# Kernel optimization log

Hardware: AMD Instinct MI355X
Metric: run time of the kernel (lower is better)

## Reference

```python
import jax, jax.numpy as jnp
import numpy as np

NUM_NODES = 10000
IN_DIM = 128
GAT_UNITS = 64
K = 20  # min(20, num_nodes - 1)
NEG_SLOPE = 0.2


def setup_inputs() -> dict:
    key = jax.random.key(0)
    ks = jax.random.split(key, 10)
    s = lambda k, shape, scale: jax.random.normal(k, shape, jnp.float32) * scale
    return {
        "x": s(ks[0], (NUM_NODES, IN_DIM), 1.0),
        "emb": s(ks[1], (NUM_NODES, 16), 1.0),
        "W1": s(ks[2], (IN_DIM, 4, GAT_UNITS), 0.05),
        "a1_src": s(ks[3], (4, GAT_UNITS), 0.05),
        "a1_tgt": s(ks[4], (4, GAT_UNITS), 0.05),
        "b1": jnp.zeros((4 * GAT_UNITS,), jnp.float32),
        "W2": s(ks[5], (4 * GAT_UNITS, 1, GAT_UNITS), 0.05),
        "a2_src": s(ks[6], (1, GAT_UNITS), 0.05),
        "a2_tgt": s(ks[7], (1, GAT_UNITS), 0.05),
        "b2": jnp.zeros((GAT_UNITS,), jnp.float32),
    }


def _build_edges(emb):
    # top-k adjacency from cosine similarity of node embeddings
    norm = emb / jnp.linalg.norm(emb, axis=-1, keepdims=True)
    sim = norm @ norm.T                      # [N, N]
    _, idx = jax.lax.top_k(sim, K)           # [N, K]
    n = emb.shape[0]
    src = jnp.repeat(jnp.arange(n, dtype=jnp.int32), K)
    tgt = idx.reshape(-1).astype(jnp.int32)
    # append self loops (as in the original module)
    loop = jnp.arange(n, dtype=jnp.int32)
    src = jnp.concatenate([src, loop])
    tgt = jnp.concatenate([tgt, loop])
    return src, tgt                          # each [N*(K+1)]


def _gat(x, W, a_src, a_tgt, src, tgt, n):
    # x: [N, F]; W: [F, H, C]; a_*: [H, C]
    h = jnp.einsum("nf,fhc->nhc", x, W)      # [N, H, C]
    e_src = jnp.einsum("nhc,hc->nh", h, a_src)  # [N, H]
    e_tgt = jnp.einsum("nhc,hc->nh", h, a_tgt)  # [N, H]
    logits = jax.nn.leaky_relu(e_src[src] + e_tgt[tgt], NEG_SLOPE)  # [E, H]
    # segment softmax over each source node's neighborhood
    m = jax.ops.segment_max(logits, src, num_segments=n)
    ex = jnp.exp(logits - m[src])
    z = jax.ops.segment_sum(ex, src, num_segments=n)
    alpha = ex / z[src]                      # [E, H]
    msg = alpha[:, :, None] * h[tgt]         # [E, H, C]
    return jax.ops.segment_sum(msg, src, num_segments=n)  # [N, H, C]


def reference(x, emb, W1, a1_src, a1_tgt, b1, W2, a2_src, a2_tgt, b2):
    n = x.shape[0]
    src, tgt = _build_edges(emb)
    # GAT layer 1: 4 heads, concatenated
    h1 = _gat(x, W1, a1_src, a1_tgt, src, tgt, n)        # [N, 4, C]
    h1 = h1.reshape(n, -1) + b1                           # [N, 4C]
    h1 = jax.nn.relu(h1)                                  # (dropout: inference mode)
    # GAT layer 2: 1 head, no concat
    h2 = _gat(h1, W2, a2_src, a2_tgt, src, tgt, n)        # [N, 1, C]
    return h2[:, 0, :] + b2                               # [N, C]
```

## Files before the change

kernel.cpp:

```cpp
#include <hip/hip_runtime.h>
#include <math.h>


#define N_NODES 10000
#define EMB_D   16
#define IN_DIM  128
#define H1      4
#define CDIM    64
#define D1      256
#define K_TOP   20
#define NEIGH   21
#define SROWS   32
#define NTILES  313
#define JSPLIT  2
#define HALFT   160
#define CAPM    96
#define GUARD   0.016f

typedef __attribute__((ext_vector_type(8)))  short short8;
typedef __attribute__((ext_vector_type(16))) float f32x16;

__device__ __forceinline__ unsigned monokey(float v) {
  unsigned u = __float_as_uint(v);
  return (u & 0x80000000u) ? ~u : (u | 0x80000000u);
}
__device__ __forceinline__ float invmono(unsigned m) {
  unsigned u = (m & 0x80000000u) ? (m ^ 0x80000000u) : ~m;
  return __uint_as_float(u);
}
__device__ __forceinline__ unsigned short f32_to_bf16(float f) {
  unsigned u = __float_as_uint(f);
  unsigned r = 0x7FFFu + ((u >> 16) & 1u);
  return (unsigned short)((u + r) >> 16);
}

__device__ __forceinline__ float dot16q(float4 qa, float4 qb, float4 qc, float4 qd,
                                        float4 v0, float4 v1, float4 v2, float4 v3) {
  float a = 0.f;
  a = fmaf(qa.x, v0.x, a); a = fmaf(qa.y, v0.y, a);
  a = fmaf(qa.z, v0.z, a); a = fmaf(qa.w, v0.w, a);
  a = fmaf(qb.x, v1.x, a); a = fmaf(qb.y, v1.y, a);
  a = fmaf(qb.z, v1.z, a); a = fmaf(qb.w, v1.w, a);
  a = fmaf(qc.x, v2.x, a); a = fmaf(qc.y, v2.y, a);
  a = fmaf(qc.z, v2.z, a); a = fmaf(qc.w, v2.w, a);
  a = fmaf(qd.x, v3.x, a); a = fmaf(qd.y, v3.y, a);
  a = fmaf(qd.z, v3.z, a); a = fmaf(qd.w, v3.w, a);
  return a;
}

__global__ __launch_bounds__(256) void normalize_kernel(
    const float* __restrict__ emb, float* __restrict__ nrm,
    unsigned short* __restrict__ nrmh) {
  int i = blockIdx.x * 256 + threadIdx.x;
  if (i >= N_NODES) return;
  const float4* p = (const float4*)(emb + (size_t)i * EMB_D);
  float4 v[4];
  float ss = 0.f;
#pragma unroll
  for (int k = 0; k < 4; k++) {
    v[k] = p[k];
    ss = fmaf(v[k].x, v[k].x, ss);
    ss = fmaf(v[k].y, v[k].y, ss);
    ss = fmaf(v[k].z, v[k].z, ss);
    ss = fmaf(v[k].w, v[k].w, ss);
  }
  float nv = sqrtf(ss);
  float4* o = (float4*)(nrm + (size_t)i * EMB_D);
  ushort4* oh = (ushort4*)(nrmh + (size_t)i * EMB_D);
#pragma unroll
  for (int k = 0; k < 4; k++) {
    float4 t;
    t.x = v[k].x / nv; t.y = v[k].y / nv; t.z = v[k].z / nv; t.w = v[k].w / nv;
    o[k] = t;
    ushort4 h;
    h.x = f32_to_bf16(t.x); h.y = f32_to_bf16(t.y);
    h.z = f32_to_bf16(t.z); h.w = f32_to_bf16(t.w);
    oh[k] = h;
  }
}

__global__ __launch_bounds__(512) void sim_topk_part(
    const float* __restrict__ nrm, const unsigned short* __restrict__ nrmh,
    unsigned long long* __restrict__ pkeys) {
  __shared__ unsigned short s_qbf[SROWS * EMB_D];
  __shared__ float s_qf[SROWS * EMB_D];
  __shared__ __align__(16) char s_ovl[32768];
  float (*s_smax)[256] = (float(*)[256])s_ovl;
  unsigned long long (*s_ckey)[CAPM] = (unsigned long long(*)[CAPM])s_ovl;
  unsigned short (*s_cid)[CAPM] =
      (unsigned short(*)[CAPM])(s_ovl + 24576);
  __shared__ float s_thr[SROWS];
  __shared__ int s_cnt[SROWS];

  int tid = threadIdx.x;
  int w = tid >> 6, lane = tid & 63;
  int lo5 = lane & 31, hi = lane >> 5;
  int row0 = blockIdx.x * SROWS;
  int bh = blockIdx.y;
  int tbase = bh * HALFT;

  if (tid < SROWS * EMB_D) {
    int gi = row0 * EMB_D + tid;
    float v = (gi < N_NODES * EMB_D) ? nrm[gi] : 0.f;
    s_qf[tid] = v;
    s_qbf[tid] = f32_to_bf16(v);
  }
  if (tid < SROWS) s_cnt[tid] = 0;
  __syncthreads();

  short8 afrag = *(const short8*)&s_qbf[lo5 * EMB_D + hi * 8];
  const f32x16 zacc = (f32x16)0.0f;

  float rm[16];
#pragma unroll
  for (int r = 0; r < 16; r++) rm[r] = -INFINITY;

#pragma unroll
  for (int g = 0; g < 5; ++g) {
    int tb = tbase + g * 32 + w * 4;
    int nd[4];
    short8 bf[4];
#pragma unroll
    for (int u = 0; u < 4; u++) {
      nd[u] = (tb + u) * 32 + lo5;
      bf[u] = (short8)(short)0;
      if (nd[u] < N_NODES)
        bf[u] = *(const short8*)&nrmh[(size_t)nd[u] * EMB_D + hi * 8];
    }
#pragma unroll
    for (int u = 0; u < 4; u++) {
      f32x16 acc = __builtin_amdgcn_mfma_f32_32x32x16_bf16(afrag, bf[u], zacc, 0, 0, 0);
      if (nd[u] < N_NODES) {
#pragma unroll
        for (int r = 0; r < 16; r++) rm[r] = fmaxf(rm[r], acc[r]);
      }
    }
  }
#pragma unroll
  for (int r = 0; r < 16; r++) {
    int rl = (r & 3) + 8 * (r >> 2) + 4 * hi;
    s_smax[rl][w * 32 + lo5] = rm[r];
  }
  __syncthreads();

  for (int q = 0; q < 4; q++) {
    int row = w * 4 + q;
    float m01 = fmaxf(s_smax[row][lane], s_smax[row][64 + lane]);
    float m23 = fmaxf(s_smax[row][128 + lane], s_smax[row][192 + lane]);
    unsigned v = monokey(fmaxf(m01, m23));
#pragma unroll
    for (int k = 2; k <= 64; k <<= 1) {
#pragma unroll
      for (int j = k >> 1; j > 0; j >>= 1) {
        unsigned o = __shfl_xor(v, j);
        bool upper = (lane & j) != 0;
        bool ascend = (lane & k) == 0;
        unsigned mx = v > o ? v : o;
        unsigned mn = v > o ? o : v;
        v = (upper == ascend) ? mx : mn;
      }
    }
    unsigned t20 = __shfl(v, 44);
    if (lane == 0)
      s_thr[row] = (row0 + row < N_NODES) ? invmono(t20) - GUARD : INFINITY;
  }
  __syncthreads();

  float thr_r[16];
#pragma unroll
  for (int r = 0; r < 16; r++)
    thr_r[r] = s_thr[(r & 3) + 8 * (r >> 2) + 4 * hi];

#pragma unroll
  for (int g = 0; g < 5; ++g) {
    int tb = tbase + g * 32 + w * 4;
    int nd[4];
    short8 bf[4];
#pragma unroll
    for (int u = 0; u < 4; u++) {
      nd[u] = (tb + u) * 32 + lo5;
      bf[u] = (short8)(short)0;
      if (nd[u] < N_NODES)
        bf[u] = *(const short8*)&nrmh[(size_t)nd[u] * EMB_D + hi * 8];
    }
#pragma unroll
    for (int u = 0; u < 4; u++) {
      f32x16 acc = __builtin_amdgcn_mfma_f32_32x32x16_bf16(afrag, bf[u], zacc, 0, 0, 0);
      if (nd[u] < N_NODES) {
#pragma unroll
        for (int r = 0; r < 16; r++) {
          if (acc[r] >= thr_r[r]) {
            int rl = (r & 3) + 8 * (r >> 2) + 4 * hi;
            int slot = atomicAdd(&s_cnt[rl], 1);
            if (slot < CAPM) s_cid[rl][slot] = (unsigned short)nd[u];
          }
        }
      }
    }
  }
  __syncthreads();

  for (int q = 0; q < 4; q++) {
    int row = w * 4 + q;
    if (row0 + row >= N_NODES) continue;
    int M = s_cnt[row];
    if (M > CAPM) continue;
    const float4* qp = (const float4*)&s_qf[row * EMB_D];
    float4 qa = qp[0], qb = qp[1], qc = qp[2], qd = qp[3];
    for (int c = lane; c < M; c += 64) {
      int id = s_cid[row][c];
      const float4* pj = (const float4*)(nrm + (size_t)id * EMB_D);
      float sim = dot16q(qa, qb, qc, qd, pj[0], pj[1], pj[2], pj[3]);
      s_ckey[row][c] = ((unsigned long long)monokey(sim) << 32) |
                       (unsigned long long)(0xFFFFFFFFu - (unsigned)id);
    }
  }
  __syncthreads();

  for (int q = 0; q < 4; q++) {
    int row = w * 4 + q;
    int grow = row0 + row;
    if (grow >= N_NODES) continue;
    unsigned long long* outp = pkeys + ((size_t)grow * JSPLIT + bh) * K_TOP;
    int M = s_cnt[row];
    if (M <= CAPM) {
      for (int c = lane; c < M; c += 64) {
        unsigned long long mykey = s_ckey[row][c];
        int rank = 0;
        for (int i = 0; i < M; i++) rank += (s_ckey[row][i] > mykey) ? 1 : 0;
        if (rank < K_TOP) outp[rank] = mykey;
      }
    } else {
      const float4* qp = (const float4*)&s_qf[row * EMB_D];
      float4 qa = qp[0], qb = qp[1], qc = qp[2], qd = qp[3];
      int j0 = tbase * 32;
      int jend = j0 + HALFT * 32; if (jend > N_NODES) jend = N_NODES;
      unsigned long long prev = ~0ull;
      for (int r = 0; r < K_TOP; r++) {
        unsigned long long best = 0ull;
        for (int j = j0 + lane; j < jend; j += 64) {
          const float4* pj = (const float4*)(nrm + (size_t)j * EMB_D);
          float sim = dot16q(qa, qb, qc, qd, pj[0], pj[1], pj[2], pj[3]);
          unsigned long long key = ((unsigned long long)monokey(sim) << 32) |
                                   (unsigned long long)(0xFFFFFFFFu - (unsigned)j);
          if (key < prev && key > best) best = key;
        }
#pragma unroll
        for (int off = 32; off > 0; off >>= 1) {
          unsigned long long o = __shfl_down(best, off);
          if (o > best) best = o;
        }
        best = __shfl(best, 0);
        prev = best;
        if (lane == 0) outp[r] = best;
      }
    }
  }
}

__global__ __launch_bounds__(256) void topk_merge(
    const unsigned long long* __restrict__ pkeys, int* __restrict__ topk) {
  __shared__ unsigned long long s_k[4][JSPLIT * K_TOP];
  int w = threadIdx.x >> 6, lane = threadIdx.x & 63;
  int row = blockIdx.x * 4 + w;
  const unsigned long long* src = pkeys + (size_t)row * (JSPLIT * K_TOP);
  if (lane < JSPLIT * K_TOP) s_k[w][lane] = src[lane];
  __syncthreads();
  if (lane < JSPLIT * K_TOP) {
    unsigned long long mykey = s_k[w][lane];
    int rank = 0;
    for (int i = 0; i < JSPLIT * K_TOP; i++)
      rank += (s_k[w][i] > mykey) ? 1 : 0;
    if (rank < K_TOP)
      topk[(size_t)row * K_TOP + rank] =
          (int)(0xFFFFFFFFu - (unsigned)(mykey & 0xFFFFFFFFull));
  }
}

__global__ __launch_bounds__(256) void gemm1_kernel(
    const float* __restrict__ A, const float* __restrict__ B,
    const float* __restrict__ a_src, const float* __restrict__ a_tgt,
    float* __restrict__ Cc, float* __restrict__ es, float* __restrict__ et) {
  __shared__ float As[16][IN_DIM];
  int r0 = blockIdx.x * 16;
  int tid = threadIdx.x;
  {
    int rr = tid >> 4;
    int kk = tid & 15;
    ((float4*)&As[rr][0])[kk] = ((const float4*)(A + (size_t)(r0 + rr) * IN_DIM))[kk];
    ((float4*)&As[rr][0])[kk + 16] =
        ((const float4*)(A + (size_t)(r0 + rr) * IN_DIM))[kk + 16];
  }
  __syncthreads();
  int y = tid >> 7;
  int c0 = (tid & 127) * 2;
  float acc[8][2] = {};
  for (int k4 = 0; k4 < IN_DIM / 4; k4++) {
    float4 a[8];
#pragma unroll
    for (int r = 0; r < 8; r++) a[r] = ((const float4*)&As[y * 8 + r][0])[k4];
    float2 bv[4];
#pragma unroll
    for (int i = 0; i < 4; i++)
      bv[i] = *(const float2*)&B[(size_t)(k4 * 4 + i) * D1 + c0];
#pragma unroll
    for (int r = 0; r < 8; r++) {
      acc[r][0] = fmaf(a[r].x, bv[0].x, acc[r][0]);
      acc[r][1] = fmaf(a[r].x, bv[0].y, acc[r][1]);
      acc[r][0] = fmaf(a[r].y, bv[1].x, acc[r][0]);
      acc[r][1] = fmaf(a[r].y, bv[1].y, acc[r][1]);
      acc[r][0] = fmaf(a[r].z, bv[2].x, acc[r][0]);
      acc[r][1] = fmaf(a[r].z, bv[2].y, acc[r][1]);
      acc[r][0] = fmaf(a[r].w, bv[3].x, acc[r][0]);
      acc[r][1] = fmaf(a[r].w, bv[3].y, acc[r][1]);
    }
  }
#pragma unroll
  for (int r = 0; r < 8; r++) {
    float2 o = {acc[r][0], acc[r][1]};
    *(float2*)&Cc[(size_t)(r0 + y * 8 + r) * D1 + c0] = o;
  }
  int lane = tid & 63;
  int h = c0 >> 6;
  float as0 = a_src[c0], as1 = a_src[c0 + 1];
  float at0 = a_tgt[c0], at1 = a_tgt[c0 + 1];
#pragma unroll
  for (int r = 0; r < 8; r++) {
    float ps = fmaf(acc[r][1], as1, acc[r][0] * as0);
    float pt = fmaf(acc[r][1], at1, acc[r][0] * at0);
#pragma unroll
    for (int off = 16; off > 0; off >>= 1) {
      ps += __shfl_down(ps, off);
      pt += __shfl_down(pt, off);
    }
    if ((lane & 31) == 0) {
      es[(size_t)(r0 + y * 8 + r) * H1 + h] = ps;
      et[(size_t)(r0 + y * 8 + r) * H1 + h] = pt;
    }
  }
}

__global__ __launch_bounds__(256) void agg1_gemm2_kernel(
    const float* __restrict__ h1p, const float* __restrict__ e1s,
    const float* __restrict__ e1t, const int* __restrict__ topk,
    const float* __restrict__ b1, const float* __restrict__ B2,
    const float* __restrict__ a_src, const float* __restrict__ a_tgt,
    float* __restrict__ h2p, float* __restrict__ es, float* __restrict__ et) {
  __shared__ float As[16][D1];
  __shared__ int nb[16][NEIGH];
  __shared__ float wv[16][NEIGH][H1];
  __shared__ float zz[16][H1];
  int r0 = blockIdx.x * 16;
  int tid = threadIdx.x;

  for (int idx = tid; idx < 16 * NEIGH; idx += 256) {
    int n = idx / NEIGH, jj = idx % NEIGH;
    nb[n][jj] = (jj < K_TOP) ? topk[(size_t)(r0 + n) * K_TOP + jj] : (r0 + n);
  }
  __syncthreads();
  for (int idx = tid; idx < 16 * NEIGH * H1; idx += 256) {
    int e = idx & 3, jj = (idx >> 2) % NEIGH, n = idx / (NEIGH * H1);
    float L = e1s[(size_t)(r0 + n) * H1 + e] + e1t[(size_t)nb[n][jj] * H1 + e];
    wv[n][jj][e] = (L > 0.f) ? L : 0.2f * L;
  }
  __syncthreads();
  if (tid < 16 * H1) {
    int n = tid >> 2, h = tid & 3;
    float m = -INFINITY;
#pragma unroll
    for (int jj = 0; jj < NEIGH; jj++) m = fmaxf(m, wv[n][jj][h]);
    float z = 0.f;
#pragma unroll
    for (int jj = 0; jj < NEIGH; jj++) {
      float wt = expf(wv[n][jj][h] - m);
      z += wt;
      wv[n][jj][h] = wt;
    }
    zz[n][h] = z;
  }
  __syncthreads();
  {
    int h = tid >> 6;
    float bv = b1[tid];
    for (int n = 0; n < 16; n++) {
      float acc = 0.f;
#pragma unroll
      for (int jj = 0; jj < NEIGH; jj++)
        acc = fmaf(wv[n][jj][h], h1p[(size_t)nb[n][jj] * D1 + tid], acc);
      float o = acc / zz[n][h] + bv;
      As[n][tid] = fmaxf(o, 0.f);
    }
  }
  __syncthreads();
  int col = tid & 63, y = tid >> 6;
  float acc4[4] = {0, 0, 0, 0};
  for (int k4 = 0; k4 < D1 / 4; k4++) {
    float4 a[4];
#pragma unroll
    for (int r = 0; r < 4; r++) a[r] = ((const float4*)&As[y * 4 + r][0])[k4];
    float bv[4];
#pragma unroll
    for (int i = 0; i < 4; i++) bv[i] = B2[(size_t)(k4 * 4 + i) * CDIM + col];
#pragma unroll
    for (int r = 0; r < 4; r++) {
      acc4[r] = fmaf(a[r].x, bv[0], acc4[r]);
      acc4[r] = fmaf(a[r].y, bv[1], acc4[r]);
      acc4[r] = fmaf(a[r].z, bv[2], acc4[r]);
      acc4[r] = fmaf(a[r].w, bv[3], acc4[r]);
    }
  }
#pragma unroll
  for (int r = 0; r < 4; r++)
    h2p[(size_t)(r0 + y * 4 + r) * CDIM + col] = acc4[r];
  float as = a_src[col], at = a_tgt[col];
#pragma unroll
  for (int r = 0; r < 4; r++) {
    float ps = acc4[r] * as, pt = acc4[r] * at;
#pragma unroll
    for (int off = 32; off > 0; off >>= 1) {
      ps += __shfl_down(ps, off);
      pt += __shfl_down(pt, off);
    }
    if (col == 0) {
      es[r0 + y * 4 + r] = ps;
      et[r0 + y * 4 + r] = pt;
    }
  }
}

__global__ __launch_bounds__(256) void agg2_kernel(
    const float* __restrict__ h2p, const float* __restrict__ es,
    const float* __restrict__ et, const int* __restrict__ topk,
    const float* __restrict__ b2, float* __restrict__ out) {
  int tid = threadIdx.x;
  int li = tid >> 6;
  int c = tid & 63;
  int i = blockIdx.x * 4 + li;
  __shared__ int nb[4][NEIGH];
  __shared__ float lg[4][NEIGH];
  if (tid < 4 * NEIGH) {
    int li2 = tid / NEIGH, jj = tid % NEIGH;
    int node = blockIdx.x * 4 + li2;
    nb[li2][jj] = (jj < K_TOP) ? topk[(size_t)node * K_TOP + jj] : node;
  }
  __syncthreads();
  if (tid < 4 * NEIGH) {
    int li2 = tid / NEIGH, jj = tid % NEIGH;
    int node = blockIdx.x * 4 + li2;
    float L = es[node] + et[nb[li2][jj]];
    lg[li2][jj] = (L > 0.f) ? L : 0.2f * L;
  }
  __syncthreads();
  float m = -INFINITY;
#pragma unroll
  for (int jj = 0; jj < NEIGH; jj++) m = fmaxf(m, lg[li][jj]);
  float z = 0.f, acc = 0.f;
#pragma unroll
  for (int jj = 0; jj < NEIGH; jj++) {
    float w = expf(lg[li][jj] - m);
    z += w;
    acc = fmaf(w, h2p[(size_t)nb[li][jj] * CDIM + c], acc);
  }
  out[(size_t)i * CDIM + c] = acc / z + b2[c];
}

extern "C" void kernel_launch(void* const* d_in, const int* in_sizes, int n_in,
                              void* d_out, int out_size, void* d_ws, size_t ws_size,
                              hipStream_t stream) {
  const float* x   = (const float*)d_in[0];
  const float* emb = (const float*)d_in[1];
  const float* W1  = (const float*)d_in[2];
  const float* a1s = (const float*)d_in[3];
  const float* a1t = (const float*)d_in[4];
  const float* b1  = (const float*)d_in[5];
  const float* W2  = (const float*)d_in[6];
  const float* a2s = (const float*)d_in[7];
  const float* a2t = (const float*)d_in[8];
  const float* b2  = (const float*)d_in[9];
  float* out = (float*)d_out;

  size_t off = 0;
  auto alloc = [&](size_t bytes) {
    void* p = (char*)d_ws + off;
    off += (bytes + 255) & ~(size_t)255;
    return p;
  };
  float*          nrm  = (float*)alloc((size_t)N_NODES * EMB_D * sizeof(float));
  unsigned short* nrmh = (unsigned short*)alloc((size_t)N_NODES * EMB_D * sizeof(unsigned short));
  int*   topk = (int*)  alloc((size_t)N_NODES * K_TOP * sizeof(int));
  float* h1p  = (float*)alloc((size_t)N_NODES * D1 * sizeof(float));
  float* e1s  = (float*)alloc((size_t)N_NODES * H1 * sizeof(float));
  float* e1t  = (float*)alloc((size_t)N_NODES * H1 * sizeof(float));
  float* h2p  = (float*)alloc((size_t)N_NODES * CDIM * sizeof(float));
  float* e2s  = (float*)alloc((size_t)N_NODES * sizeof(float));
  float* e2t  = (float*)alloc((size_t)N_NODES * sizeof(float));
  unsigned long long* pkeys = (unsigned long long*)h1p;
  (void)ws_size; (void)in_sizes; (void)n_in; (void)out_size;

  normalize_kernel<<<(N_NODES + 255) / 256, 256, 0, stream>>>(emb, nrm, nrmh);
  sim_topk_part<<<dim3(NTILES, JSPLIT), 512, 0, stream>>>(nrm, nrmh, pkeys);
  topk_merge<<<N_NODES / 4, 256, 0, stream>>>(pkeys, topk);
  gemm1_kernel<<<N_NODES / 16, 256, 0, stream>>>(x, W1, a1s, a1t, h1p, e1s, e1t);
  agg1_gemm2_kernel<<<N_NODES / 16, 256, 0, stream>>>(h1p, e1s, e1t, topk, b1,
                                                      W2, a2s, a2t, h2p, e2s, e2t);
  agg2_kernel<<<N_NODES / 4, 256, 0, stream>>>(h2p, e2s, e2t, topk, b2, out);
}
```

Measured before the change: 139.3 us.

## Move candidate rescoring and ranking from similarity kernel into merge kernel

```diff
diff --git a/kernel.cpp b/kernel.cpp
--- a/kernel.cpp
+++ b/kernel.cpp
@@ -81,14 +81,10 @@
 
 __global__ __launch_bounds__(512) void sim_topk_part(
     const float* __restrict__ nrm, const unsigned short* __restrict__ nrmh,
-    unsigned long long* __restrict__ pkeys) {
+    unsigned short* __restrict__ cids, int* __restrict__ cnts) {
   __shared__ unsigned short s_qbf[SROWS * EMB_D];
   __shared__ float s_qf[SROWS * EMB_D];
-  __shared__ __align__(16) char s_ovl[32768];
-  float (*s_smax)[256] = (float(*)[256])s_ovl;
-  unsigned long long (*s_ckey)[CAPM] = (unsigned long long(*)[CAPM])s_ovl;
-  unsigned short (*s_cid)[CAPM] =
-      (unsigned short(*)[CAPM])(s_ovl + 24576);
+  __shared__ float s_smax[SROWS][256];
   __shared__ float s_thr[SROWS];
   __shared__ int s_cnt[SROWS];
 
@@ -192,27 +188,12 @@
           if (acc[r] >= thr_r[r]) {
             int rl = (r & 3) + 8 * (r >> 2) + 4 * hi;
             int slot = atomicAdd(&s_cnt[rl], 1);
-            if (slot < CAPM) s_cid[rl][slot] = (unsigned short)nd[u];
+            if (slot < CAPM)
+              cids[((size_t)(row0 + rl) * JSPLIT + bh) * CAPM + slot] =
+                  (unsigned short)nd[u];
           }
         }
       }
-    }
-  }
-  __syncthreads();
-
-  for (int q = 0; q < 4; q++) {
-    int row = w * 4 + q;
-    if (row0 + row >= N_NODES) continue;
-    int M = s_cnt[row];
-    if (M > CAPM) continue;
-    const float4* qp = (const float4*)&s_qf[row * EMB_D];
-    float4 qa = qp[0], qb = qp[1], qc = qp[2], qd = qp[3];
-    for (int c = lane; c < M; c += 64) {
-      int id = s_cid[row][c];
-      const float4* pj = (const float4*)(nrm + (size_t)id * EMB_D);
-      float sim = dot16q(qa, qb, qc, qd, pj[0], pj[1], pj[2], pj[3]);
-      s_ckey[row][c] = ((unsigned long long)monokey(sim) << 32) |
-                       (unsigned long long)(0xFFFFFFFFu - (unsigned)id);
     }
   }
   __syncthreads();
@@ -221,16 +202,11 @@
     int row = w * 4 + q;
     int grow = row0 + row;
     if (grow >= N_NODES) continue;
-    unsigned long long* outp = pkeys + ((size_t)grow * JSPLIT + bh) * K_TOP;
     int M = s_cnt[row];
     if (M <= CAPM) {
-      for (int c = lane; c < M; c += 64) {
-        unsigned long long mykey = s_ckey[row][c];
-        int rank = 0;
-        for (int i = 0; i < M; i++) rank += (s_ckey[row][i] > mykey) ? 1 : 0;
-        if (rank < K_TOP) outp[rank] = mykey;
-      }
+      if (lane == 0) cnts[grow * JSPLIT + bh] = M;
     } else {
+      unsigned short* outc = cids + ((size_t)grow * JSPLIT + bh) * CAPM;
       const float4* qp = (const float4*)&s_qf[row * EMB_D];
       float4 qa = qp[0], qb = qp[1], qc = qp[2], qd = qp[3];
       int j0 = tbase * 32;
@@ -252,25 +228,39 @@
         }
         best = __shfl(best, 0);
         prev = best;
-        if (lane == 0) outp[r] = best;
+        if (lane == 0)
+          outc[r] = (unsigned short)(0xFFFFFFFFu - (unsigned)(best & 0xFFFFFFFFull));
       }
+      if (lane == 0) cnts[grow * JSPLIT + bh] = K_TOP;
     }
   }
 }
 
 __global__ __launch_bounds__(256) void topk_merge(
-    const unsigned long long* __restrict__ pkeys, int* __restrict__ topk) {
-  __shared__ unsigned long long s_k[4][JSPLIT * K_TOP];
+    const float* __restrict__ nrm, const unsigned short* __restrict__ cids,
+    const int* __restrict__ cnts, int* __restrict__ topk) {
+  __shared__ unsigned long long s_k[4][JSPLIT * CAPM];
   int w = threadIdx.x >> 6, lane = threadIdx.x & 63;
   int row = blockIdx.x * 4 + w;
-  const unsigned long long* src = pkeys + (size_t)row * (JSPLIT * K_TOP);
-  if (lane < JSPLIT * K_TOP) s_k[w][lane] = src[lane];
-  __syncthreads();
-  if (lane < JSPLIT * K_TOP) {
-    unsigned long long mykey = s_k[w][lane];
+  int M1 = cnts[row * JSPLIT + 0];
+  int M2 = cnts[row * JSPLIT + 1];
+  int M = M1 + M2;
+  const float4* qp = (const float4*)(nrm + (size_t)row * EMB_D);
+  float4 qa = qp[0], qb = qp[1], qc = qp[2], qd = qp[3];
+  const unsigned short* c0 = cids + ((size_t)row * JSPLIT + 0) * CAPM;
+  const unsigned short* c1 = cids + ((size_t)row * JSPLIT + 1) * CAPM;
+  for (int c = lane; c < M; c += 64) {
+    int id = (c < M1) ? c0[c] : c1[c - M1];
+    const float4* pj = (const float4*)(nrm + (size_t)id * EMB_D);
+    float sim = dot16q(qa, qb, qc, qd, pj[0], pj[1], pj[2], pj[3]);
+    s_k[w][c] = ((unsigned long long)monokey(sim) << 32) |
+                (unsigned long long)(0xFFFFFFFFu - (unsigned)id);
+  }
+  __syncthreads();
+  for (int c = lane; c < M; c += 64) {
+    unsigned long long mykey = s_k[w][c];
     int rank = 0;
-    for (int i = 0; i < JSPLIT * K_TOP; i++)
-      rank += (s_k[w][i] > mykey) ? 1 : 0;
+    for (int i = 0; i < M; i++) rank += (s_k[w][i] > mykey) ? 1 : 0;
     if (rank < K_TOP)
       topk[(size_t)row * K_TOP + rank] =
           (int)(0xFFFFFFFFu - (unsigned)(mykey & 0xFFFFFFFFull));
@@ -494,12 +484,13 @@
   float* h2p  = (float*)alloc((size_t)N_NODES * CDIM * sizeof(float));
   float* e2s  = (float*)alloc((size_t)N_NODES * sizeof(float));
   float* e2t  = (float*)alloc((size_t)N_NODES * sizeof(float));
-  unsigned long long* pkeys = (unsigned long long*)h1p;
+  unsigned short* cids = (unsigned short*)h1p;
+  int* cnts = (int*)((char*)h1p + (size_t)N_NODES * JSPLIT * CAPM * sizeof(unsigned short));
   (void)ws_size; (void)in_sizes; (void)n_in; (void)out_size;
 
   normalize_kernel<<<(N_NODES + 255) / 256, 256, 0, stream>>>(emb, nrm, nrmh);
-  sim_topk_part<<<dim3(NTILES, JSPLIT), 512, 0, stream>>>(nrm, nrmh, pkeys);
-  topk_merge<<<N_NODES / 4, 256, 0, stream>>>(pkeys, topk);
+  sim_topk_part<<<dim3(NTILES, JSPLIT), 512, 0, stream>>>(nrm, nrmh, cids, cnts);
+  topk_merge<<<N_NODES / 4, 256, 0, stream>>>(nrm, cids, cnts, topk);
   gemm1_kernel<<<N_NODES / 16, 256, 0, stream>>>(x, W1, a1s, a1t, h1p, e1s, e1t);
   agg1_gemm2_kernel<<<N_NODES / 16, 256, 0, stream>>>(h1p, e1s, e1t, topk, b1,
                                                       W2, a2s, a2t, h2p, e2s, e2t);
```

Result: no change. 140.5 us (+0.9%).
